# Optimization experiments

Hardware: AMD Instinct MI355X
Metric: run time of the kernel (lower is better)

## Reference

```python
import jax, jax.numpy as jnp
import numpy as np
import math

C_S = 384; C_Z = 128; C_H = 16; H = 12; PQ = 4; PV = 8; C_SURF = 16
N_RES = 512; N_SURF = 2048; B = 1
INF = 1e5; EPS = 1e-8
SOFTPLUS_INV_1 = 0.541324854612918


def _quat_to_rot(q):
    q = q / jnp.linalg.norm(q, axis=-1, keepdims=True)
    w, x, y, z = q[..., 0], q[..., 1], q[..., 2], q[..., 3]
    R = jnp.stack([
        1 - 2 * (y * y + z * z), 2 * (x * y - w * z), 2 * (x * z + w * y),
        2 * (x * y + w * z), 1 - 2 * (x * x + z * z), 2 * (y * z - w * x),
        2 * (x * z - w * y), 2 * (y * z + w * x), 1 - 2 * (x * x + y * y),
    ], axis=-1)
    return R.reshape(q.shape[:-1] + (3, 3))


def setup_inputs() -> dict:
    key = jax.random.key(0)
    ks = jax.random.split(key, 32)
    hc = H * C_H            # 192
    hpq = H * PQ * 3        # 144
    hpkv = H * (PQ + PV) * 3  # 432
    cz4 = C_Z // 4
    concat = hc + H * PV * 3 + H * PV + H * cz4 + hc  # 1152
    w = lambda k, i, o: jax.random.normal(k, (i, o), jnp.float32) * 0.02
    inp = {
        's': jax.random.normal(ks[0], (B, N_RES, C_S), jnp.float32),
        'z': jax.random.normal(ks[1], (B, N_RES, N_RES, C_Z), jnp.float32),
        'rots': _quat_to_rot(jax.random.normal(ks[2], (B, N_RES, 4), jnp.float32)),
        'trans': jax.random.normal(ks[3], (B, N_RES, 3), jnp.float32) * 10.0,
        'mask': jnp.ones((B, N_RES), jnp.float32),
        'surface_points': jax.random.normal(ks[4], (B, N_SURF, 3), jnp.float32) * 10.0,
        'surface_features': jax.random.normal(ks[5], (B, N_SURF, C_SURF), jnp.float32),
        'surface_mask': jnp.ones((B, N_SURF), jnp.float32),
        'Wq': w(ks[6], C_S, hc), 'bq': jnp.zeros((hc,)),
        'Wkv': w(ks[7], C_S, 2 * hc), 'bkv': jnp.zeros((2 * hc,)),
        'Wqp': w(ks[8], C_S, hpq), 'bqp': jnp.zeros((hpq,)),
        'Wkvp': w(ks[9], C_S, hpkv), 'bkvp': jnp.zeros((hpkv,)),
        'Wse': w(ks[10], C_SURF, C_S), 'bse': jnp.zeros((C_S,)),
        'Wsq': w(ks[11], C_S, hc), 'bsq': jnp.zeros((hc,)),
        'Wsk': w(ks[12], C_S, hc), 'bsk': jnp.zeros((hc,)),
        'Wsv': w(ks[13], C_S, hc), 'bsv': jnp.zeros((hc,)),
        'Wb': w(ks[14], C_Z, H), 'bb': jnp.zeros((H,)),
        'Wdz': w(ks[15], C_Z, cz4), 'bdz': jnp.zeros((cz4,)),
        'head_weights': jnp.full((H,), SOFTPLUS_INV_1, jnp.float32),
        'sb_weights': jnp.full((1,), SOFTPLUS_INV_1, jnp.float32),
        'Wout': w(ks[16], concat, C_S), 'bout': jnp.zeros((C_S,)),
        'Wso': w(ks[17], 2 * C_S, C_SURF), 'bso': jnp.zeros((C_SURF,)),
    }
    return inp


def reference(s, z, rots, trans, mask, surface_points, surface_features, surface_mask,
              Wq, bq, Wkv, bkv, Wqp, bqp, Wkvp, bkvp, Wse, bse, Wsq, bsq, Wsk, bsk,
              Wsv, bsv, Wb, bb, Wdz, bdz, head_weights, sb_weights, Wout, bout, Wso, bso):
    lin = lambda x, W, b: x @ W + b
    b_, n, _ = s.shape
    m = surface_points.shape[-2]

    surface_feat = lin(surface_features, Wse, bse)                    # [B,M,c_s]
    # backbone<->surface squared distances
    disp = trans[:, :, None, :] - surface_points[:, None, :, :]       # [B,N,M,3]
    dist_sq = jnp.sum(disp * disp, -1)                                # [B,N,M]

    q = lin(s, Wq, bq).reshape(b_, n, H, C_H)
    kv = lin(s, Wkv, bkv).reshape(b_, n, H, 2 * C_H)
    k, v = kv[..., :C_H], kv[..., C_H:]

    # query points: split into 3 coord chunks, stack, rigid-apply
    qp = lin(s, Wqp, bqp)
    qp = jnp.stack(jnp.split(qp, 3, axis=-1), axis=-1)                # [B,N,H*PQ,3]
    qp = jnp.einsum('bnij,bnpj->bnpi', rots, qp) + trans[:, :, None]
    qp = qp.reshape(b_, n, H, PQ, 3)

    kvp = lin(s, Wkvp, bkvp)
    kvp = jnp.stack(jnp.split(kvp, 3, axis=-1), axis=-1)              # [B,N,H*(PQ+PV),3]
    kvp = jnp.einsum('bnij,bnpj->bnpi', rots, kvp) + trans[:, :, None]
    kvp = kvp.reshape(b_, n, H, PQ + PV, 3)
    kp, vp = kvp[..., :PQ, :], kvp[..., PQ:, :]

    b_bias = lin(z, Wb, bb)                                           # [B,N,N,H]
    a = jnp.einsum('bihc,bjhc->bhij', q, k) * math.sqrt(1.0 / (3 * C_H))
    a = a + math.sqrt(1.0 / 3) * jnp.transpose(b_bias, (0, 3, 1, 2))

    # point-distance attention term
    pt = jnp.sum((qp[:, :, None] - kp[:, None]) ** 2, axis=-1)        # [B,N,N,H,PQ]
    hw = jax.nn.softplus(head_weights)                                # [H]
    pt = jnp.sum(pt, axis=-1) * hw * math.sqrt(1.0 / (3 * (PQ * 9.0 / 2))) * (-0.5)
    a = a + jnp.transpose(pt, (0, 3, 1, 2))                           # [B,H,N,N]

    sq_mask = INF * (mask[:, :, None] * mask[:, None, :] - 1.0)
    a = jax.nn.softmax(a + sq_mask[:, None], axis=-1)

    o = jnp.einsum('bhij,bjhc->bihc', a, v).reshape(b_, n, H * C_H)
    o_pt = jnp.einsum('bhij,bjhpd->bihpd', a, vp)                     # [B,N,H,PV,3]
    o_pt = jnp.einsum('bnji,bnhpj->bnhpi', rots, o_pt - trans[:, :, None, None])
    o_pt_norm = jnp.sqrt(jnp.sum(o_pt ** 2, -1) + EPS).reshape(b_, n, H * PV)
    o_pt_flat = o_pt.reshape(b_, n, H * PV, 3)

    pair_z = lin(z, Wdz, bdz)                                         # [B,N,N,cz/4]
    o_pair = jnp.einsum('bhij,bijc->bihc', a, pair_z).reshape(b_, n, -1)

    # surface cross-attention branch
    sq = lin(s, Wsq, bsq).reshape(b_, n, H, C_H)
    sk = lin(surface_feat, Wsk, bsk).reshape(b_, m, H, C_H)
    sv = lin(surface_feat, Wsv, bsv).reshape(b_, m, H, C_H)
    logits = jnp.einsum('bnhc,bmhc->bhnm', sq, sk) * math.sqrt(1.0 / C_H)
    sbw = jax.nn.softplus(sb_weights)[0]
    logits = logits - 0.5 * sbw * dist_sq[:, None]
    cross_mask = mask[:, :, None] * surface_mask[:, None, :]          # [B,N,M]
    logits = logits + INF * (cross_mask - 1.0)[:, None]
    a_s = jax.nn.softmax(logits, axis=-1)
    o_surf = jnp.einsum('bhnm,bmhc->bnhc', a_s, sv).reshape(b_, n, H * C_H)

    o_cat = jnp.concatenate([o, o_pt_flat[..., 0], o_pt_flat[..., 1], o_pt_flat[..., 2],
                             o_pt_norm, o_pair, o_surf], axis=-1)
    s_out = lin(o_cat, Wout, bout)                                    # [B,N,c_s]

    # surface update: attend surface points to backbone (softmax over residues)
    a_ts = jax.nn.softmax(jnp.swapaxes(logits, -1, -2), axis=-1).mean(axis=1)  # [B,M,N]
    s_agg = jnp.einsum('bmn,bnc->bmc', a_ts, s)
    surf_out = lin(jnp.concatenate([surface_feat, s_agg], axis=-1), Wso, bso)
    return s_out, surf_out
```

## Files before the change

kernel.cpp:

```cpp
#include <hip/hip_runtime.h>
#include <cstddef>


#define CS 384
#define INFV 100000.0f

__device__ __forceinline__ float softplusf(float x) { return log1pf(__expf(x)); }

__global__ __launch_bounds__(256) void k_pack(
    const float* __restrict__ Wq, const float* __restrict__ Wsq,
    const float* __restrict__ Wkv, const float* __restrict__ Wqp,
    const float* __restrict__ Wkvp, const float* __restrict__ Wsk,
    const float* __restrict__ Wsv, const float* __restrict__ Wout,
    const float* __restrict__ bq, const float* __restrict__ bsq,
    const float* __restrict__ bkv, const float* __restrict__ bqp,
    const float* __restrict__ bkvp, const float* __restrict__ bsk,
    const float* __restrict__ bsv,
    float* __restrict__ wt1, float* __restrict__ wt2, float* __restrict__ wt3,
    float* __restrict__ b1, float* __restrict__ b2)
{
    const int b = blockIdx.x, t = threadIdx.x;
    if (b >= 1092) {
        int idx = (b - 1092) * 256 + t;
        if (idx < 1344) {
            float v;
            if (idx < 192) v = bq[idx];
            else if (idx < 384) v = bsq[idx - 192];
            else if (idx < 768) v = bkv[idx - 384];
            else if (idx < 912) v = bqp[idx - 768];
            else v = bkvp[idx - 912];
            b1[idx] = v;
        } else if (idx < 1728) {
            int i2 = idx - 1344;
            b2[i2] = (i2 < 192) ? bsk[i2] : bsv[i2 - 192];
        }
        return;
    }
    const float* src; float* dst; int C, coff, tile, ldd;
    if (b < 72)       { src = Wq;   C = 192; dst = wt1; coff = 0;   ldd = 384;  tile = b; }
    else if (b < 144) { src = Wsq;  C = 192; dst = wt1; coff = 192; ldd = 384;  tile = b - 72; }
    else if (b < 288) { src = Wkv;  C = 384; dst = wt1; coff = 384; ldd = 384;  tile = b - 144; }
    else if (b < 348) { src = Wqp;  C = 144; dst = wt1; coff = 768; ldd = 384;  tile = b - 288; }
    else if (b < 516) { src = Wkvp; C = 432; dst = wt1; coff = 912; ldd = 384;  tile = b - 348; }
    else if (b < 588) { src = Wsk;  C = 192; dst = wt2; coff = 0;   ldd = 384;  tile = b - 516; }
    else if (b < 660) { src = Wsv;  C = 192; dst = wt2; coff = 192; ldd = 384;  tile = b - 588; }
    else              { src = Wout; C = 384; dst = wt3; coff = 0;   ldd = 1152; tile = b - 660; }
    const int cT = (C + 31) >> 5;
    const int tk = tile / cT, tc = tile % cT;
    __shared__ float l[32][33];
    const int tr = t >> 5, tcc = t & 31;
    #pragma unroll
    for (int rr = 0; rr < 4; ++rr) {
        int kloc = tr * 4 + rr;
        int cg = tc * 32 + tcc;
        l[kloc][tcc] = (cg < C) ? src[(size_t)(tk * 32 + kloc) * C + cg] : 0.f;
    }
    __syncthreads();
    #pragma unroll
    for (int rr = 0; rr < 4; ++rr) {
        int cloc = tr * 4 + rr;
        int cg = tc * 32 + cloc;
        if (cg < C) dst[(size_t)(coff + cg) * ldd + tk * 32 + tcc] = l[tcc][cloc];
    }
}

__global__ __launch_bounds__(256) void k_packz(
    const float* __restrict__ Wb, const float* __restrict__ bb,
    const float* __restrict__ Wdz, const float* __restrict__ bdz,
    float* __restrict__ wz, float* __restrict__ bz)
{
    const float s3 = 0.5773502691896258f;
    int idx = blockIdx.x * 256 + threadIdx.x;
    if (idx < 5632) {
        int c = idx >> 7, kk = idx & 127;
        wz[idx] = (c < 12) ? s3 * Wb[kk * 12 + c] : Wdz[kk * 32 + (c - 12)];
    } else if (idx < 5676) {
        int c = idx - 5632;
        bz[c] = (c < 12) ? s3 * bb[c] : bdz[c - 12];
    }
}

__global__ __launch_bounds__(256) void k_transp(
    const float* __restrict__ A, float* __restrict__ At)
{
    __shared__ float tile[32][33];
    const int r0 = blockIdx.y * 32, c0 = blockIdx.x * 32;
    const int tr = threadIdx.x >> 5, tc = threadIdx.x & 31;
    #pragma unroll
    for (int rr = 0; rr < 4; ++rr)
        tile[tr + rr * 8][tc] = A[(size_t)(r0 + tr + rr * 8) * 384 + c0 + tc];
    __syncthreads();
    #pragma unroll
    for (int rr = 0; rr < 4; ++rr)
        At[(size_t)(c0 + tr + rr * 8) * 512 + r0 + tc] = tile[tc][tr + rr * 8];
}

template<int KTOT, bool HB>
__global__ __launch_bounds__(256) void k_gemm(
    const float* __restrict__ A, const float* __restrict__ Wt,
    const float* __restrict__ bias, float* __restrict__ C, int ldc)
{
    __shared__ float As[64][68];
    __shared__ float Ws[64][68];
    const int t = threadIdx.x;
    const int c0 = blockIdx.x * 64, m0 = blockIdx.y * 64;
    const int sr = t >> 4, sk4 = (t & 15) << 2;
    const int wid = t >> 6, lane = t & 63;
    const int wr = (wid >> 1) * 32, wc = (wid & 1) * 32;
    const int lr = lane >> 3, lc = lane & 7;
    float acc[4][4];
    #pragma unroll
    for (int j = 0; j < 4; ++j) {
        float bv = HB ? bias[c0 + wc + lc + 8 * j] : 0.f;
        #pragma unroll
        for (int i = 0; i < 4; ++i) acc[i][j] = bv;
    }
    for (int kc = 0; kc < KTOT; kc += 64) {
        __syncthreads();
        #pragma unroll
        for (int rep = 0; rep < 4; ++rep) {
            int row = sr + rep * 16;
            *(float4*)&As[row][sk4] = *(const float4*)&A[(size_t)(m0 + row) * KTOT + kc + sk4];
            *(float4*)&Ws[row][sk4] = *(const float4*)&Wt[(size_t)(c0 + row) * KTOT + kc + sk4];
        }
        __syncthreads();
        #pragma unroll 4
        for (int k4 = 0; k4 < 16; ++k4) {
            float4 a[4], w[4];
            #pragma unroll
            for (int i = 0; i < 4; ++i) a[i] = *(float4*)&As[wr + lr + 8 * i][k4 * 4];
            #pragma unroll
            for (int j = 0; j < 4; ++j) w[j] = *(float4*)&Ws[wc + lc + 8 * j][k4 * 4];
            #pragma unroll
            for (int i = 0; i < 4; ++i) {
                #pragma unroll
                for (int j = 0; j < 4; ++j) {
                    acc[i][j] = fmaf(a[i].x, w[j].x, acc[i][j]);
                    acc[i][j] = fmaf(a[i].y, w[j].y, acc[i][j]);
                    acc[i][j] = fmaf(a[i].z, w[j].z, acc[i][j]);
                    acc[i][j] = fmaf(a[i].w, w[j].w, acc[i][j]);
                }
            }
        }
    }
    #pragma unroll
    for (int i = 0; i < 4; ++i) {
        #pragma unroll
        for (int j = 0; j < 4; ++j)
            C[(size_t)(m0 + wr + lr + 8 * i) * ldc + c0 + wc + lc + 8 * j] = acc[i][j];
    }
}

__global__ __launch_bounds__(256) void k_scatter(
    const float* __restrict__ proj, const float* __restrict__ rots,
    const float* __restrict__ trans,
    float* __restrict__ qw, float* __restrict__ kw, float* __restrict__ vw,
    float* __restrict__ sqw, float* __restrict__ qpw, float* __restrict__ kpw,
    float* __restrict__ vpw)
{
    __shared__ float p[4][1344];
    const int n0 = blockIdx.x * 4, t = threadIdx.x;
    for (int idx = t; idx < 1344; idx += 256) {
        #pragma unroll
        for (int r = 0; r < 4; ++r) p[r][idx] = proj[(size_t)(n0 + r) * 1344 + idx];
    }
    __syncthreads();
    for (int idx = t; idx < 3072; idx += 256) {
        int r = idx / 768, c = idx % 768;
        int n = n0 + r;
        float v = p[r][c];
        if (c < 192) qw[(size_t)n * 192 + c] = v;
        else if (c < 384) sqw[(size_t)n * 192 + (c - 192)] = v;
        else {
            int cc = c - 384, h = cc >> 5, sub = cc & 31;
            if (sub < 16) kw[(size_t)n * 192 + h * 16 + sub] = v;
            else          vw[(size_t)n * 192 + h * 16 + (sub - 16)] = v;
        }
    }
    for (int idx = t; idx < 2304; idx += 256) {
        int r = idx / 576, rem = idx % 576;
        int n = n0 + r;
        const float* R = &rots[(size_t)n * 9];
        const float* tr = &trans[(size_t)n * 3];
        if (rem < 144) {
            int pp = rem / 3, d = rem % 3;
            float v = fmaf(R[d*3+0], p[r][768 + pp],
                      fmaf(R[d*3+1], p[r][768 + 48 + pp],
                      fmaf(R[d*3+2], p[r][768 + 96 + pp], tr[d])));
            qpw[(size_t)n * 144 + pp * 3 + d] = v;
        } else {
            int rem2 = rem - 144; int pp = rem2 / 3, d = rem2 % 3;
            float v = fmaf(R[d*3+0], p[r][912 + pp],
                      fmaf(R[d*3+1], p[r][912 + 144 + pp],
                      fmaf(R[d*3+2], p[r][912 + 288 + pp], tr[d])));
            int h = pp / 12, ii = pp % 12;
            if (ii < 4) kpw[(size_t)n * 144 + h * 12 + ii * 3 + d] = v;
            else        vpw[(size_t)n * 288 + h * 24 + (ii - 4) * 3 + d] = v;
        }
    }
}

__global__ __launch_bounds__(256) void k_sfeat(
    const float* __restrict__ sf, const float* __restrict__ Wse,
    const float* __restrict__ bse, float* __restrict__ sfeat)
{
    __shared__ float wl[16 * 384];
    __shared__ float sfl[8][16];
    const int m0 = blockIdx.x * 8, t = threadIdx.x;
    for (int idx = t; idx < 6144; idx += 256) wl[idx] = Wse[idx];
    if (t < 128) sfl[t >> 4][t & 15] = sf[(size_t)(m0 + (t >> 4)) * 16 + (t & 15)];
    __syncthreads();
    #pragma unroll
    for (int u = 0; u < 12; ++u) {
        int idx = t + u * 256;
        int r = idx / 384, c = idx % 384;
        float a = bse[c];
        #pragma unroll
        for (int kk = 0; kk < 16; ++kk) a = fmaf(sfl[r][kk], wl[kk * 384 + c], a);
        sfeat[(size_t)(m0 + r) * 384 + c] = a;
    }
}

__global__ __launch_bounds__(256) void k_zpass(
    const float* __restrict__ z, const float* __restrict__ wz,
    const float* __restrict__ bz, float* __restrict__ bpz)
{
    __shared__ float zt[64][132];
    __shared__ float wt[44 * 128];
    const int t = threadIdx.x;
    const int jg0 = blockIdx.x * 64;
    const int i = jg0 >> 9;
    const int jloc = jg0 & 511;
    const int jl = t & 63;
    const int cgs = __builtin_amdgcn_readfirstlane(t >> 6);
    #pragma unroll
    for (int u = 0; u < 6; ++u) {
        int idx = t + u * 256;
        if (idx < 1408) *(float4*)&wt[idx * 4] = *(const float4*)&wz[idx * 4];
    }
    #pragma unroll
    for (int u = 0; u < 8; ++u) {
        int idx = t + u * 256;
        int r = idx >> 5, c4 = (idx & 31) << 2;
        *(float4*)&zt[r][c4] = *(const float4*)&z[((size_t)(jg0 + r)) * 128 + c4];
    }
    float bv[11];
    #pragma unroll
    for (int u = 0; u < 11; ++u) bv[u] = bz[cgs * 11 + u];
    __syncthreads();
    float acc[11];
    #pragma unroll
    for (int u = 0; u < 11; ++u) acc[u] = bv[u];
    const float* wbase = &wt[cgs * 11 * 128];
    #pragma unroll 4
    for (int k4 = 0; k4 < 128; k4 += 4) {
        float4 zv = *(float4*)&zt[jl][k4];
        float4 wv[11];
        #pragma unroll
        for (int u = 0; u < 11; ++u)
            wv[u] = *(const float4*)&wbase[u * 128 + k4];
        #pragma unroll
        for (int u = 0; u < 11; ++u) {
            acc[u] = fmaf(zv.x, wv[u].x, acc[u]);
            acc[u] = fmaf(zv.y, wv[u].y, acc[u]);
            acc[u] = fmaf(zv.z, wv[u].z, acc[u]);
            acc[u] = fmaf(zv.w, wv[u].w, acc[u]);
        }
    }
    #pragma unroll
    for (int u = 0; u < 11; ++u)
        bpz[((size_t)i * 44 + cgs * 11 + u) * 512 + jloc + jl] = acc[u];
}

__global__ __launch_bounds__(256) void k_attn_a(
    const float* __restrict__ qw, const float* __restrict__ kw,
    const float* __restrict__ qpw, const float* __restrict__ kpw,
    const float* __restrict__ bpz, const float* __restrict__ mask,
    const float* __restrict__ hwp, float* __restrict__ abuf)
{
    __shared__ float pls[4][520];
    __shared__ float qs[64], qps[48], cpt4[4];
    const int i = blockIdx.x, hg = blockIdx.y;
    const int t = threadIdx.x;
    if (t < 64) qs[t] = qw[(size_t)i * 192 + hg * 64 + t];
    if (t < 48) qps[t] = qpw[(size_t)i * 144 + hg * 48 + t];
    if (t < 4) cpt4[t] = -0.5f * 0.13608276348795434f * softplusf(hwp[hg * 4 + t]);
    const float mask_i = mask[i];
    __syncthreads();
    #pragma unroll 2
    for (int it = 0; it < 8; ++it) {
        int idx = t + it * 256;
        int hh = idx >> 9, j = idx & 511;
        int h = hg * 4 + hh;
        float kj[16], kpj[12];
        { const float4* kr = (const float4*)&kw[(size_t)j * 192 + h * 16];
          *(float4*)&kj[0] = kr[0]; *(float4*)&kj[4] = kr[1];
          *(float4*)&kj[8] = kr[2]; *(float4*)&kj[12] = kr[3]; }
        { const float4* kr = (const float4*)&kpw[(size_t)j * 144 + h * 12];
          *(float4*)&kpj[0] = kr[0]; *(float4*)&kpj[4] = kr[1]; *(float4*)&kpj[8] = kr[2]; }
        float qk = 0.f;
        #pragma unroll
        for (int c = 0; c < 16; ++c) qk = fmaf(qs[hh * 16 + c], kj[c], qk);
        float pts = 0.f;
        #pragma unroll
        for (int p = 0; p < 4; ++p) {
            float dx = qps[hh*12+p*3+0] - kpj[p*3+0];
            float dy = qps[hh*12+p*3+1] - kpj[p*3+1];
            float dz = qps[hh*12+p*3+2] - kpj[p*3+2];
            pts += dx*dx + dy*dy + dz*dz;
        }
        float lg = fmaf(0.14433756729740643f, qk, bpz[((size_t)i * 44 + h) * 512 + j]);
        lg = fmaf(cpt4[hh], pts, lg);
        lg += INFV * (mask_i * mask[j] - 1.0f);
        pls[hh][j] = lg;
    }
    __syncthreads();
    const int w = t >> 6, lane = t & 63;
    float v[8];
    #pragma unroll
    for (int k = 0; k < 8; ++k) v[k] = pls[w][lane + k * 64];
    float mx = v[0];
    #pragma unroll
    for (int k = 1; k < 8; ++k) mx = fmaxf(mx, v[k]);
    #pragma unroll
    for (int off = 32; off; off >>= 1) mx = fmaxf(mx, __shfl_xor(mx, off));
    float sm = 0.f;
    #pragma unroll
    for (int k = 0; k < 8; ++k) { v[k] = __expf(v[k] - mx); sm += v[k]; }
    #pragma unroll
    for (int off = 32; off; off >>= 1) sm += __shfl_xor(sm, off);
    const float inv = 1.0f / sm;
    float* dst = abuf + ((size_t)(hg * 4 + w) * 512 + i) * 512;
    #pragma unroll
    for (int k = 0; k < 8; ++k) dst[lane + k * 64] = v[k] * inv;
}

__global__ __launch_bounds__(256) void k_attn_pair(
    const float* __restrict__ abuf, const float* __restrict__ bpz,
    float* __restrict__ ocat)
{
    __shared__ float al[12][512];
    const int i = blockIdx.x, t = threadIdx.x;
    #pragma unroll
    for (int u = 0; u < 12; ++u) {
        al[u][t] = abuf[(size_t)u * 262144 + (size_t)i * 512 + t];
        al[u][t + 256] = abuf[(size_t)u * 262144 + (size_t)i * 512 + t + 256];
    }
    __syncthreads();
    const int c = t & 31;
    const int h1 = t >> 5;
    const bool dual = (t < 128);
    const float* pz = bpz + ((size_t)i * 44 + 12 + c) * 512;
    const float* a1 = al[h1];
    const float* a2 = al[dual ? h1 + 8 : 0];
    float acc1 = 0.f, acc2 = 0.f;
    for (int j = 0; j < 512; j += 4) {
        float4 p = *(const float4*)&pz[j];
        acc1 = fmaf(a1[j+0], p.x, acc1);
        acc1 = fmaf(a1[j+1], p.y, acc1);
        acc1 = fmaf(a1[j+2], p.z, acc1);
        acc1 = fmaf(a1[j+3], p.w, acc1);
        if (dual) {
            acc2 = fmaf(a2[j+0], p.x, acc2);
            acc2 = fmaf(a2[j+1], p.y, acc2);
            acc2 = fmaf(a2[j+2], p.z, acc2);
            acc2 = fmaf(a2[j+3], p.w, acc2);
        }
    }
    ocat[(size_t)i * 1152 + 576 + h1 * 32 + c] = acc1;
    if (dual) ocat[(size_t)i * 1152 + 576 + (h1 + 8) * 32 + c] = acc2;
}

__global__ __launch_bounds__(256) void k_gemm_ov(
    const float* __restrict__ abuf, const float* __restrict__ vw,
    const float* __restrict__ vpw, float* __restrict__ cbuf)
{
    __shared__ float As[64][68];
    __shared__ float Bs[64][44];
    const int i0 = blockIdx.x * 64, h = blockIdx.y;
    const int t = threadIdx.x;
    const int sr = t >> 4, sk4 = (t & 15) << 2;
    const int r1 = t >> 3;
    const int cb = t & 7;
    float acc[2][5];
    #pragma unroll
    for (int u = 0; u < 5; ++u) { acc[0][u] = 0.f; acc[1][u] = 0.f; }
    for (int kc = 0; kc < 512; kc += 64) {
        __syncthreads();
        #pragma unroll
        for (int rep = 0; rep < 4; ++rep) {
            int row = sr + rep * 16;
            *(float4*)&As[row][sk4] =
                *(const float4*)&abuf[(size_t)h * 262144 + (size_t)(i0 + row) * 512 + kc + sk4];
        }
        #pragma unroll
        for (int u = 0; u < 10; ++u) {
            int idx = t + u * 256;
            int r = idx / 40, cc = idx % 40;
            Bs[r][cc] = (cc < 16) ? vw[(size_t)(kc + r) * 192 + h * 16 + cc]
                                  : vpw[(size_t)(kc + r) * 288 + h * 24 + (cc - 16)];
        }
        __syncthreads();
        #pragma unroll 4
        for (int kk = 0; kk < 64; ++kk) {
            float av1 = As[r1][kk], av2 = As[r1 + 32][kk];
            #pragma unroll
            for (int u = 0; u < 5; ++u) {
                float b = Bs[kk][cb + 8 * u];
                acc[0][u] = fmaf(av1, b, acc[0][u]);
                acc[1][u] = fmaf(av2, b, acc[1][u]);
            }
        }
    }
    #pragma unroll
    for (int u = 0; u < 5; ++u) {
        cbuf[((size_t)h * 512 + i0 + r1) * 40 + cb + 8 * u] = acc[0][u];
        cbuf[((size_t)h * 512 + i0 + r1 + 32) * 40 + cb + 8 * u] = acc[1][u];
    }
}

__global__ __launch_bounds__(256) void k_optfin(
    const float* __restrict__ cbuf, const float* __restrict__ rots,
    const float* __restrict__ trans, float* __restrict__ ocat)
{
    __shared__ float cl[4][12][40];
    const int i0 = blockIdx.x * 4, t = threadIdx.x;
    for (int idx = t; idx < 1920; idx += 256) {
        int ii = idx / 480, rem = idx % 480;
        int h = rem / 40, c = rem % 40;
        cl[ii][h][c] = cbuf[((size_t)h * 512 + i0 + ii) * 40 + c];
    }
    __syncthreads();
    for (int idx = t; idx < 768; idx += 256) {
        int ii = idx / 192, o = idx % 192;
        ocat[(size_t)(i0 + ii) * 1152 + o] = cl[ii][o >> 4][o & 15];
    }
    for (int idx = t; idx < 384; idx += 256) {
        int ii = idx / 96, hp = idx % 96;
        int h = hp >> 3, p = hp & 7;
        int i = i0 + ii;
        const float* R = &rots[(size_t)i * 9];
        float gx = cl[ii][h][16 + p*3 + 0] - trans[(size_t)i*3 + 0];
        float gy = cl[ii][h][16 + p*3 + 1] - trans[(size_t)i*3 + 1];
        float gz = cl[ii][h][16 + p*3 + 2] - trans[(size_t)i*3 + 2];
        float lx = R[0]*gx + R[3]*gy + R[6]*gz;
        float ly = R[1]*gx + R[4]*gy + R[7]*gz;
        float lz = R[2]*gx + R[5]*gy + R[8]*gz;
        float nm = sqrtf(lx*lx + ly*ly + lz*lz + 1e-8f);
        int col = h * 8 + p;
        size_t base = (size_t)i * 1152;
        ocat[base + 192 + col] = lx;
        ocat[base + 288 + col] = ly;
        ocat[base + 384 + col] = lz;
        ocat[base + 480 + col] = nm;
    }
}

__global__ __launch_bounds__(256) void k_tlog(
    const float* __restrict__ sqw, const float* __restrict__ skv,
    const float* __restrict__ trans, const float* __restrict__ mask,
    const float* __restrict__ sp, const float* __restrict__ smask,
    const float* __restrict__ sbwp, float* __restrict__ logits,
    float* __restrict__ stat_m, float* __restrict__ stat_il)
{
    __shared__ float sk_s[32][16];
    __shared__ float sq_s[32][16];
    __shared__ float trans_s[96];
    __shared__ float mask_s[32];
    __shared__ float spm_s[96];
    __shared__ float smask_s[32];
    const int h = blockIdx.y;
    const int m0 = blockIdx.x * 32;
    const int t = threadIdx.x;
    const int tmg = t >> 5, tnl = t & 31;
    const float sbw = softplusf(sbwp[0]);
    for (int idx = t; idx < 512; idx += 256) {
        int row = idx >> 4, c = idx & 15;
        sk_s[row][c] = skv[(size_t)(m0 + row) * 384 + h * 16 + c];
    }
    if (t < 96) spm_s[t] = sp[(size_t)m0 * 3 + t];
    if (t < 32) smask_s[t] = smask[m0 + t];
    __syncthreads();
    float skr[4][16];
    float spx[4], spy[4], spz[4], smk[4];
    #pragma unroll
    for (int mi = 0; mi < 4; ++mi) {
        int row = tmg * 4 + mi;
        #pragma unroll
        for (int c4 = 0; c4 < 16; c4 += 4)
            *(float4*)&skr[mi][c4] = *(float4*)&sk_s[row][c4];
        spx[mi] = spm_s[row*3+0]; spy[mi] = spm_s[row*3+1]; spz[mi] = spm_s[row*3+2];
        smk[mi] = smask_s[row];
    }
    float mxr[4], lr[4];
    #pragma unroll
    for (int mi = 0; mi < 4; ++mi) { mxr[mi] = -1e30f; lr[mi] = 0.f; }
    for (int nt = 0; nt < 16; ++nt) {
        __syncthreads();
        const int nb = nt * 32;
        if (t < 128) {
            int nn = t >> 2, c4 = (t & 3) << 2;
            *(float4*)&sq_s[nn][c4] = *(const float4*)&sqw[(size_t)(nb + nn) * 192 + h * 16 + c4];
        }
        if (t < 96) trans_s[t] = trans[(size_t)nb * 3 + t];
        if (t < 32) mask_s[t] = mask[nb + t];
        __syncthreads();
        float q[16];
        #pragma unroll
        for (int c4 = 0; c4 < 16; c4 += 4)
            *(float4*)&q[c4] = *(float4*)&sq_s[tnl][c4];
        const float tx = trans_s[tnl*3+0], ty = trans_s[tnl*3+1], tz = trans_s[tnl*3+2];
        const float mkn = mask_s[tnl];
        #pragma unroll
        for (int mi = 0; mi < 4; ++mi) {
            float dot = 0.f;
            #pragma unroll
            for (int c = 0; c < 16; ++c) dot = fmaf(skr[mi][c], q[c], dot);
            float dx = tx - spx[mi], dy = ty - spy[mi], dz = tz - spz[mi];
            float mterm = INFV * (mkn * smk[mi] - 1.0f) - 0.5f * sbw * (dx*dx + dy*dy + dz*dz);
            float lg = fmaf(0.25f, dot, mterm);
            logits[((size_t)(m0 + tmg * 4 + mi) * 12 + h) * 512 + nb + tnl] = lg;
            float newm = fmaxf(mxr[mi], lg);
            lr[mi] = lr[mi] * __expf(mxr[mi] - newm) + __expf(lg - newm);
            mxr[mi] = newm;
        }
    }
    #pragma unroll
    for (int off = 1; off < 32; off <<= 1) {
        #pragma unroll
        for (int mi = 0; mi < 4; ++mi) {
            float m2 = __shfl_xor(mxr[mi], off), l2 = __shfl_xor(lr[mi], off);
            float newm = fmaxf(mxr[mi], m2);
            lr[mi] = lr[mi] * __expf(mxr[mi] - newm) + l2 * __expf(m2 - newm);
            mxr[mi] = newm;
        }
    }
    if (tnl == 0) {
        #pragma unroll
        for (int mi = 0; mi < 4; ++mi) {
            int m = m0 + tmg * 4 + mi;
            stat_m[(size_t)m * 12 + h] = mxr[mi];
            stat_il[(size_t)m * 12 + h] = 1.0f / lr[mi];
        }
    }
}

__global__ __launch_bounds__(256) void k_rstat(
    const float* __restrict__ lbuf, float* __restrict__ rspm,
    float* __restrict__ rsps)
{
    __shared__ float smx[4][64], ssm[4][64];
    const int n0 = blockIdx.x * 64, mc = blockIdx.y, h = blockIdx.z;
    const int t = threadIdx.x, ln = t & 63, mg = t >> 6;
    const int mb = mc * 512;
    const int n = n0 + ln;
    float mx = -1e30f, sm = 0.f;
    #pragma unroll 2
    for (int it = 0; it < 128; ++it) {
        int m = mb + it * 4 + mg;
        float lg = lbuf[((size_t)m * 12 + h) * 512 + n];
        float nm = fmaxf(mx, lg);
        sm = sm * __expf(mx - nm) + __expf(lg - nm);
        mx = nm;
    }
    smx[mg][ln] = mx; ssm[mg][ln] = sm;
    __syncthreads();
    if (t < 64) {
        float M = smx[0][t], S = ssm[0][t];
        #pragma unroll
        for (int g = 1; g < 4; ++g) {
            float m2 = smx[g][t], s2 = ssm[g][t];
            float nm = fmaxf(M, m2);
            S = S * __expf(M - nm) + s2 * __expf(m2 - nm);
            M = nm;
        }
        rspm[((size_t)h * 4 + mc) * 512 + n0 + t] = M;
        rsps[((size_t)h * 4 + mc) * 512 + n0 + t] = S;
    }
}

__global__ __launch_bounds__(256) void k_rcomb(
    const float* __restrict__ rspm, const float* __restrict__ rsps,
    float* __restrict__ rmax, float* __restrict__ rinv)
{
    int gid = blockIdx.x * 256 + threadIdx.x;
    if (gid >= 6144) return;
    int h = gid >> 9, n = gid & 511;
    float M = -1e30f, S = 0.f;
    #pragma unroll
    for (int mc = 0; mc < 4; ++mc) {
        float m2 = rspm[((size_t)h * 4 + mc) * 512 + n];
        float s2 = rsps[((size_t)h * 4 + mc) * 512 + n];
        float nm = fmaxf(M, m2);
        S = S * __expf(M - nm) + s2 * __expf(m2 - nm);
        M = nm;
    }
    rmax[gid] = M;
    rinv[gid] = 1.0f / S;
}

__global__ __launch_bounds__(256) void k_pv(
    const float* __restrict__ lbuf, const float* __restrict__ skv,
    const float* __restrict__ rmax, const float* __restrict__ rinv,
    float* __restrict__ pvp)
{
    __shared__ float sv_s[512][17];
    const int n0 = blockIdx.x * 64, mc = blockIdx.y, h = blockIdx.z;
    const int t = threadIdx.x, ln = t & 63, mg = t >> 6;
    const int mb = mc * 512;
    for (int idx = t; idx < 2048; idx += 256) {
        int ml = idx >> 2, c4 = (idx & 3) << 2;
        float4 v4 = *(const float4*)&skv[(size_t)(mb + ml) * 384 + 192 + h * 16 + c4];
        sv_s[ml][c4+0]=v4.x; sv_s[ml][c4+1]=v4.y; sv_s[ml][c4+2]=v4.z; sv_s[ml][c4+3]=v4.w;
    }
    const int n = n0 + ln;
    const float rm = rmax[h * 512 + n], ri = rinv[h * 512 + n];
    float acc[16];
    #pragma unroll
    for (int c = 0; c < 16; ++c) acc[c] = 0.f;
    __syncthreads();
    #pragma unroll 2
    for (int it = 0; it < 128; ++it) {
        int ml = it * 4 + mg;
        float w = __expf(lbuf[((size_t)(mb + ml) * 12 + h) * 512 + n] - rm) * ri;
        #pragma unroll
        for (int c = 0; c < 16; ++c) acc[c] = fmaf(w, sv_s[ml][c], acc[c]);
    }
    __syncthreads();
    float* red = &sv_s[0][0];
    #pragma unroll
    for (int c = 0; c < 16; ++c) red[(mg * 64 + ln) * 17 + c] = acc[c];
    __syncthreads();
    {
        int nl = t >> 2, c4 = (t & 3) << 2;
        float4 o;
        #pragma unroll
        for (int e = 0; e < 4; ++e) {
            float s = 0.f;
            #pragma unroll
            for (int g = 0; g < 4; ++g) s += red[(g * 64 + nl) * 17 + c4 + e];
            (&o.x)[e] = s;
        }
        *(float4*)&pvp[(((size_t)h * 4 + mc) * 512 + n0 + nl) * 16 + c4] = o;
    }
}

__global__ __launch_bounds__(256) void k_pvcomb(
    const float* __restrict__ pvp, float* __restrict__ ocat)
{
    int gid = blockIdx.x * 256 + threadIdx.x;
    int n = gid / 192, rem = gid % 192;
    float o = 0.f;
    #pragma unroll
    for (int mc = 0; mc < 4; ++mc)
        o += pvp[(((size_t)(rem >> 4) * 4 + mc) * 512 + n) * 16 + (rem & 15)];
    ocat[(size_t)n * 1152 + 960 + rem] = o;
}

__global__ __launch_bounds__(256) void k_tw(
    const float* __restrict__ logits, const float* __restrict__ stat_m,
    const float* __restrict__ stat_il, float* __restrict__ w)
{
    __shared__ float mxs[12], ils[12];
    const int m = blockIdx.x, t = threadIdx.x;
    if (t < 12) { mxs[t] = stat_m[(size_t)m * 12 + t]; ils[t] = stat_il[(size_t)m * 12 + t]; }
    __syncthreads();
    const float* lp = logits + (size_t)m * 12 * 512;
    float a0 = 0.f, a1 = 0.f;
    #pragma unroll
    for (int h = 0; h < 12; ++h) {
        a0 += __expf(lp[h * 512 + t] - mxs[h]) * ils[h];
        a1 += __expf(lp[h * 512 + 256 + t] - mxs[h]) * ils[h];
    }
    w[(size_t)m * 512 + t] = a0 * (1.0f / 12.0f);
    w[(size_t)m * 512 + 256 + t] = a1 * (1.0f / 12.0f);
}

__global__ __launch_bounds__(256) void k_surf_out(
    const float* __restrict__ sfeat, const float* __restrict__ saggw,
    const float* __restrict__ Wso, const float* __restrict__ bso,
    float* __restrict__ out)
{
    __shared__ float wl[12304];
    const int t = threadIdx.x;
    for (int idx = t; idx < 12288; idx += 256) {
        int k = idx >> 4, c = idx & 15;
        wl[(k / 192) * 3076 + (k % 192) * 16 + c] = Wso[idx];
    }
    const int m = blockIdx.x * 64 + (t >> 2);
    const int kq = t & 3;
    const float* src = (kq < 2) ? &sfeat[(size_t)m * 384 + kq * 192]
                                : &saggw[(size_t)m * 384 + (kq - 2) * 192];
    __syncthreads();
    float acc[16];
    #pragma unroll
    for (int c = 0; c < 16; ++c) acc[c] = 0.f;
    const float* wb = &wl[kq * 3076];
    for (int k = 0; k < 192; k += 4) {
        float4 v = *(const float4*)&src[k];
        #pragma unroll
        for (int e = 0; e < 4; ++e) {
            float sv = (&v.x)[e];
            #pragma unroll
            for (int c = 0; c < 16; ++c)
                acc[c] = fmaf(sv, wb[(k + e) * 16 + c], acc[c]);
        }
    }
    #pragma unroll
    for (int c = 0; c < 16; ++c) {
        acc[c] += __shfl_xor(acc[c], 1);
        acc[c] += __shfl_xor(acc[c], 2);
    }
    #pragma unroll
    for (int c = 0; c < 16; ++c) {
        if ((c >> 2) == kq) out[196608 + (size_t)m * 16 + c] = acc[c] + bso[c];
    }
}

extern "C" void kernel_launch(void* const* d_in, const int* in_sizes, int n_in,
                              void* d_out, int out_size, void* d_ws, size_t ws_size,
                              hipStream_t stream)
{
    (void)in_sizes; (void)n_in; (void)out_size; (void)ws_size;
    const float* s     = (const float*)d_in[0];
    const float* z     = (const float*)d_in[1];
    const float* rots  = (const float*)d_in[2];
    const float* trans = (const float*)d_in[3];
    const float* mask  = (const float*)d_in[4];
    const float* sp    = (const float*)d_in[5];
    const float* sf    = (const float*)d_in[6];
    const float* smask = (const float*)d_in[7];
    const float* Wq    = (const float*)d_in[8];  const float* bq   = (const float*)d_in[9];
    const float* Wkv   = (const float*)d_in[10]; const float* bkv  = (const float*)d_in[11];
    const float* Wqp   = (const float*)d_in[12]; const float* bqp  = (const float*)d_in[13];
    const float* Wkvp  = (const float*)d_in[14]; const float* bkvp = (const float*)d_in[15];
    const float* Wse   = (const float*)d_in[16]; const float* bse  = (const float*)d_in[17];
    const float* Wsq   = (const float*)d_in[18]; const float* bsq  = (const float*)d_in[19];
    const float* Wsk   = (const float*)d_in[20]; const float* bsk  = (const float*)d_in[21];
    const float* Wsv   = (const float*)d_in[22]; const float* bsv  = (const float*)d_in[23];
    const float* Wb    = (const float*)d_in[24]; const float* bb   = (const float*)d_in[25];
    const float* Wdz   = (const float*)d_in[26]; const float* bdz  = (const float*)d_in[27];
    const float* hw    = (const float*)d_in[28]; const float* sbw  = (const float*)d_in[29];
    const float* Wout  = (const float*)d_in[30]; const float* bout = (const float*)d_in[31];
    const float* Wso   = (const float*)d_in[32]; const float* bso  = (const float*)d_in[33];
    float* out = (float*)d_out;

    float* qw    = (float*)d_ws;
    float* kw    = qw    + (size_t)512 * 192;
    float* vw    = kw    + (size_t)512 * 192;
    float* sqw   = vw    + (size_t)512 * 192;
    float* qpw   = sqw   + (size_t)512 * 192;
    float* kpw   = qpw   + (size_t)512 * 144;
    float* vpw   = kpw   + (size_t)512 * 144;
    float* sfeat = vpw   + (size_t)512 * 288;
    float* skv   = sfeat + (size_t)2048 * 384;
    float* ocat  = skv   + (size_t)2048 * 384;
    float* sagg  = ocat  + (size_t)512 * 1152;
    float* region = sagg + (size_t)2048 * 384;
    float* proj   = region;
    float* bpz    = region;
    float* logits = region;
    float* wt1   = region + (size_t)2048 * 12 * 512;
    float* wt2   = wt1   + (size_t)1344 * 384;
    float* wt3   = wt2   + (size_t)384 * 384;
    float* b1    = wt3   + (size_t)384 * 1152;
    float* b2    = b1    + 1344;
    float* st    = b2    + 384;
    float* wbuf  = st    + (size_t)384 * 512;
    float* statm = wbuf  + (size_t)2048 * 512;
    float* stati = statm + (size_t)2048 * 12;
    float* abuf  = stati + (size_t)2048 * 12;
    float* cbuf  = abuf  + (size_t)12 * 512 * 512;
    float* wz    = cbuf  + (size_t)12 * 512 * 40;
    float* bz    = wz    + (size_t)44 * 128;
    float* rspm  = bz    + 64;
    float* rsps  = rspm  + (size_t)12 * 4 * 512;
    float* rmax  = rsps  + (size_t)12 * 4 * 512;
    float* rinv  = rmax  + (size_t)12 * 512;
    float* pvp   = rinv  + (size_t)12 * 512;

    k_pack<<<dim3(1099), dim3(256), 0, stream>>>(Wq, Wsq, Wkv, Wqp, Wkvp, Wsk, Wsv, Wout,
        bq, bsq, bkv, bqp, bkvp, bsk, bsv, wt1, wt2, wt3, b1, b2);
    k_packz<<<dim3(23), dim3(256), 0, stream>>>(Wb, bb, Wdz, bdz, wz, bz);
    k_transp<<<dim3(12, 16), dim3(256), 0, stream>>>(s, st);
    k_gemm<384, true><<<dim3(21, 8), dim3(256), 0, stream>>>(s, wt1, b1, proj, 1344);
    k_scatter<<<dim3(128), dim3(256), 0, stream>>>(proj, rots, trans,
        qw, kw, vw, sqw, qpw, kpw, vpw);
    k_sfeat<<<dim3(256), dim3(256), 0, stream>>>(sf, Wse, bse, sfeat);
    k_gemm<384, true><<<dim3(6, 32), dim3(256), 0, stream>>>(sfeat, wt2, b2, skv, 384);
    k_zpass<<<dim3(4096), dim3(256), 0, stream>>>(z, wz, bz, bpz);
    k_attn_a<<<dim3(512, 3), dim3(256), 0, stream>>>(qw, kw, qpw, kpw, bpz, mask, hw, abuf);
    k_attn_pair<<<dim3(512), dim3(256), 0, stream>>>(abuf, bpz, ocat);
    k_gemm_ov<<<dim3(8, 12), dim3(256), 0, stream>>>(abuf, vw, vpw, cbuf);
    k_optfin<<<dim3(128), dim3(256), 0, stream>>>(cbuf, rots, trans, ocat);
    k_tlog<<<dim3(64, 12), dim3(256), 0, stream>>>(sqw, skv, trans, mask, sp, smask,
        sbw, logits, statm, stati);
    k_rstat<<<dim3(8, 4, 12), dim3(256), 0, stream>>>(logits, rspm, rsps);
    k_rcomb<<<dim3(24), dim3(256), 0, stream>>>(rspm, rsps, rmax, rinv);
    k_pv<<<dim3(8, 4, 12), dim3(256), 0, stream>>>(logits, skv, rmax, rinv, pvp);
    k_pvcomb<<<dim3(384), dim3(256), 0, stream>>>(pvp, ocat);
    k_tw<<<dim3(2048), dim3(256), 0, stream>>>(logits, statm, stati, wbuf);
    k_gemm<512, false><<<dim3(6, 32), dim3(256), 0, stream>>>(wbuf, st, nullptr, sagg, 384);
    k_surf_out<<<dim3(32), dim3(256), 0, stream>>>(sfeat, sagg, Wso, bso, out);
    k_gemm<1152, true><<<dim3(6, 8), dim3(256), 0, stream>>>(ocat, wt3, bout, out, 384);
}
```

Baseline: 549.4 us.

## Retile z projection kernel to 128 rows per block with K-chunked shared memory

Measured after the change: 530.0 us. -3.5%, faster.

```diff
diff --git a/kernel.cpp b/kernel.cpp
--- a/kernel.cpp
+++ b/kernel.cpp
@@ -225,51 +225,58 @@
     const float* __restrict__ z, const float* __restrict__ wz,
     const float* __restrict__ bz, float* __restrict__ bpz)
 {
-    __shared__ float zt[64][132];
-    __shared__ float wt[44 * 128];
+    __shared__ float zt[128][68];
+    __shared__ float wt[44][64];
     const int t = threadIdx.x;
-    const int jg0 = blockIdx.x * 64;
+    const int jg0 = blockIdx.x * 128;
     const int i = jg0 >> 9;
     const int jloc = jg0 & 511;
     const int jl = t & 63;
     const int cgs = __builtin_amdgcn_readfirstlane(t >> 6);
-    #pragma unroll
-    for (int u = 0; u < 6; ++u) {
-        int idx = t + u * 256;
-        if (idx < 1408) *(float4*)&wt[idx * 4] = *(const float4*)&wz[idx * 4];
-    }
-    #pragma unroll
-    for (int u = 0; u < 8; ++u) {
-        int idx = t + u * 256;
-        int r = idx >> 5, c4 = (idx & 31) << 2;
-        *(float4*)&zt[r][c4] = *(const float4*)&z[((size_t)(jg0 + r)) * 128 + c4];
-    }
-    float bv[11];
-    #pragma unroll
-    for (int u = 0; u < 11; ++u) bv[u] = bz[cgs * 11 + u];
-    __syncthreads();
-    float acc[11];
-    #pragma unroll
-    for (int u = 0; u < 11; ++u) acc[u] = bv[u];
-    const float* wbase = &wt[cgs * 11 * 128];
-    #pragma unroll 4
-    for (int k4 = 0; k4 < 128; k4 += 4) {
-        float4 zv = *(float4*)&zt[jl][k4];
-        float4 wv[11];
-        #pragma unroll
-        for (int u = 0; u < 11; ++u)
-            wv[u] = *(const float4*)&wbase[u * 128 + k4];
-        #pragma unroll
-        for (int u = 0; u < 11; ++u) {
-            acc[u] = fmaf(zv.x, wv[u].x, acc[u]);
-            acc[u] = fmaf(zv.y, wv[u].y, acc[u]);
-            acc[u] = fmaf(zv.z, wv[u].z, acc[u]);
-            acc[u] = fmaf(zv.w, wv[u].w, acc[u]);
-        }
-    }
-    #pragma unroll
-    for (int u = 0; u < 11; ++u)
-        bpz[((size_t)i * 44 + cgs * 11 + u) * 512 + jloc + jl] = acc[u];
+    float acc[2][11];
+    #pragma unroll
+    for (int u = 0; u < 11; ++u) {
+        float b = bz[cgs * 11 + u];
+        acc[0][u] = b; acc[1][u] = b;
+    }
+    for (int kc = 0; kc < 128; kc += 64) {
+        __syncthreads();
+        for (int idx = t; idx < 704; idx += 256) {
+            int c = idx >> 4, k4 = (idx & 15) << 2;
+            *(float4*)&wt[c][k4] = *(const float4*)&wz[c * 128 + kc + k4];
+        }
+        #pragma unroll
+        for (int u = 0; u < 8; ++u) {
+            int idx = t + u * 256;
+            int r = idx >> 4, k4 = (idx & 15) << 2;
+            *(float4*)&zt[r][k4] = *(const float4*)&z[((size_t)(jg0 + r)) * 128 + kc + k4];
+        }
+        __syncthreads();
+        const float* wbase = &wt[cgs * 11][0];
+        #pragma unroll 4
+        for (int k4 = 0; k4 < 64; k4 += 4) {
+            float4 z0 = *(float4*)&zt[jl][k4];
+            float4 z1 = *(float4*)&zt[jl + 64][k4];
+            #pragma unroll
+            for (int u = 0; u < 11; ++u) {
+                float4 wv = *(const float4*)&wbase[u * 64 + k4];
+                acc[0][u] = fmaf(z0.x, wv.x,
+                            fmaf(z0.y, wv.y,
+                            fmaf(z0.z, wv.z,
+                            fmaf(z0.w, wv.w, acc[0][u]))));
+                acc[1][u] = fmaf(z1.x, wv.x,
+                            fmaf(z1.y, wv.y,
+                            fmaf(z1.z, wv.z,
+                            fmaf(z1.w, wv.w, acc[1][u]))));
+            }
+        }
+    }
+    #pragma unroll
+    for (int u = 0; u < 11; ++u) {
+        size_t base = ((size_t)i * 44 + cgs * 11 + u) * 512 + jloc;
+        bpz[base + jl] = acc[0][u];
+        bpz[base + 64 + jl] = acc[1][u];
+    }
 }
 
 __global__ __launch_bounds__(256) void k_attn_a(
@@ -788,7 +795,7 @@
         qw, kw, vw, sqw, qpw, kpw, vpw);
     k_sfeat<<<dim3(256), dim3(256), 0, stream>>>(sf, Wse, bse, sfeat);
     k_gemm<384, true><<<dim3(6, 32), dim3(256), 0, stream>>>(sfeat, wt2, b2, skv, 384);
-    k_zpass<<<dim3(4096), dim3(256), 0, stream>>>(z, wz, bz, bpz);
+    k_zpass<<<dim3(2048), dim3(256), 0, stream>>>(z, wz, bz, bpz);
     k_attn_a<<<dim3(512, 3), dim3(256), 0, stream>>>(qw, kw, qpw, kpw, bpz, mask, hw, abuf);
     k_attn_pair<<<dim3(512), dim3(256), 0, stream>>>(abuf, bpz, ocat);
     k_gemm_ov<<<dim3(8, 12), dim3(256), 0, stream>>>(abuf, vw, vpw, cbuf);
```
